# Kernel tuning notes

Hardware: AMD Instinct MI355X
Metric: run time of the kernel (lower is better)

The kernel has to match this reference:

```python
import jax, jax.numpy as jnp
import numpy as np
from jax import lax

ALPHA = 100.0      # SuperSpike surrogate slope (LIFParameters alpha)
DT = 1e-3          # norse default dt
TAU_SYN_INV = 200.0
TAU_MEM_INV = 100.0
V_TH = 1.0

@jax.custom_vjp
def superspike(x):
    return (x > 0).astype(x.dtype)

def _ss_fwd(x):
    return (x > 0).astype(x.dtype), x

def _ss_bwd(x, g):
    return (g / (ALPHA * jnp.abs(x) + 1.0) ** 2,)

superspike.defvjp(_ss_fwd, _ss_bwd)

def lif_step(inp, v, i):
    # norse lif_step: decay v/i, spike on v_decayed - v_th, reset, then add input current
    v_dec = v + DT * TAU_MEM_INV * (-v + i)
    i_dec = i * (1.0 - DT * TAU_SYN_INV)
    z = superspike(v_dec - V_TH)
    v_new = (1.0 - z) * v_dec  # v_reset = 0
    i_new = i_dec + inp
    return z, v_new, i_new

def li_step(inp, v, i):
    # leaky integrator readout (LILinearCell): returns membrane voltage
    v_new = v + DT * TAU_MEM_INV * (-v + i)
    i_new = i * (1.0 - DT * TAU_SYN_INV) + inp
    return v_new, v_new, i_new

def conv2d(x, w, b):
    y = lax.conv_general_dilated(x, w, (1, 1), 'VALID',
                                 dimension_numbers=('NCHW', 'OIHW', 'NCHW'))
    return y + b[None, :, None, None]

def maxpool2(x):
    return lax.reduce_window(x, -jnp.inf, lax.max, (1, 1, 2, 2), (1, 1, 2, 2), 'VALID')

def setup_inputs() -> dict:
    key = jax.random.key(0)
    ks = jax.random.split(key, 9)
    T, B, C, H = 16, 64, 3, 64
    feats = int(((H - 4) / 2 - 4) / 2)  # 13
    def unif(k, shape, fan_in):
        bound = 1.0 / np.sqrt(fan_in)
        return jax.random.uniform(k, shape, jnp.float32, -bound, bound)
    return {
        'x':  jax.random.normal(ks[0], (T, B, C, H, H), jnp.float32),
        'w1': unif(ks[1], (32, C, 5, 5), C * 25),
        'b1': unif(ks[2], (32,), C * 25),
        'w2': unif(ks[3], (64, 32, 5, 5), 32 * 25),
        'b2': unif(ks[4], (64,), 32 * 25),
        'wf': unif(ks[5], (1024, feats * feats * 64), feats * feats * 64),
        'bf': unif(ks[6], (1024,), feats * feats * 64),
        'wo': unif(ks[7], (10, 1024), 1024),
        'bo': unif(ks[8], (10,), 1024),
    }

def reference(x, w1, b1, w2, b2, wf, bf, wo, bo):
    T, B, C, H, _ = x.shape
    h1 = H - 4           # conv1 out spatial
    p1 = h1 // 2         # pool1
    h2 = p1 - 4          # conv2 out spatial
    p2 = h2 // 2         # pool2 (== features)
    dtype = x.dtype
    zeros = lambda s: jnp.zeros(s, dtype)
    carry0 = (zeros((B, 32, h1, h1)), zeros((B, 32, h1, h1)),   # lif0 v, i
              zeros((B, 64, h2, h2)), zeros((B, 64, h2, h2)),   # lif1 v, i
              zeros((B, 1024)), zeros((B, 1024)),               # lif2 v, i
              zeros((B, 10)), zeros((B, 10)))                   # out  v, i

    def step(carry, xt):
        v0, i0, v1, i1, v2, i2, vo, io = carry
        z = conv2d(xt, w1, b1)
        z, v0, i0 = lif_step(z, v0, i0)
        z = maxpool2(z)
        z = 10.0 * conv2d(z, w2, b2)
        z, v1, i1 = lif_step(z, v1, i1)
        z = maxpool2(z)
        z = z.reshape(B, -1)
        z = z @ wf.T + bf
        z, v2, i2 = lif_step(z, v2, i2)
        inp = jax.nn.relu(z) @ wo.T + bo
        v, vo, io = li_step(inp, vo, io)
        return (v0, i0, v1, i1, v2, i2, vo, io), v

    _, voltages = lax.scan(step, carry0, x)
    return voltages  # [T, B, 10]
```

## Files before the change

kernel.cpp:

```cpp
#include <hip/hip_runtime.h>

typedef __attribute__((ext_vector_type(8))) short short8v;
typedef __attribute__((ext_vector_type(4))) float f32x4;

#define DT_TM 0.1f
#define SYN_DEC 0.8f
#define TT 16
#define BB 64
#define FCK 10816

#define BO_S1   ((size_t)0)
#define BO_S2   ((size_t)29491200)
#define BO_S3   ((size_t)51642368)
#define BO_PART ((size_t)55836672)
#define BO_WH2  BO_PART
#define BO_WL2  (BO_PART + 102400)
#define BO_AFW  (BO_PART + 204800)
#define BO_WHF  ((size_t)72613888)
#define BO_WLF  ((size_t)94765056)
#define BIG_NEED ((size_t)116916224)

#define FO_S1   ((size_t)0)
#define FO_S2   ((size_t)29491200)
#define FO_S3   ((size_t)40566784)
#define FO_PART ((size_t)44761088)
#define FO_V2   ((size_t)51576832)
#define FO_I2   ((size_t)51838976)
#define FO_WH2  FO_PART
#define FO_WL2  (FO_PART + 102400)

__device__ __forceinline__ unsigned short bf16_rne(float f) {
  unsigned int u = __float_as_uint(f);
  return (unsigned short)((u + 0x7FFFu + ((u >> 16) & 1u)) >> 16);
}

__global__ __launch_bounds__(256) void k0_prep(
    const float* __restrict__ w2, unsigned short* __restrict__ whi,
    unsigned short* __restrict__ wlo) {
  int e = blockIdx.x * 256 + threadIdx.x;
  if (e >= 25 * 64 * 32) return;
  int kk = e >> 11;
  int rem = e & 2047;
  int oc = rem >> 5, c = rem & 31;
  float w = w2[(size_t)(oc * 32 + c) * 25 + kk];
  unsigned short hi = bf16_rne(w);
  float fhi = __uint_as_float((unsigned int)hi << 16);
  unsigned short lo = bf16_rne(w - fhi);
  whi[e] = hi;
  wlo[e] = lo;
}

__global__ __launch_bounds__(256) void k0b_wf(
    const float* __restrict__ wf, unsigned short* __restrict__ whiF,
    unsigned short* __restrict__ wloF) {
  size_t e = (size_t)blockIdx.x * 256 + threadIdx.x;
  if (e >= (size_t)1024 * FCK) return;
  float w = wf[e];
  unsigned short hi = bf16_rne(w);
  float fhi = __uint_as_float((unsigned int)hi << 16);
  whiF[e] = hi;
  wloF[e] = bf16_rne(w - fhi);
}

__global__ __launch_bounds__(256) void k0w_prep(
    const float* __restrict__ w1, unsigned short* __restrict__ afw) {
  int e = blockIdx.x * 256 + threadIdx.x;
  if (e >= 9216) return;
  int i = e & 7, l = (e >> 3) & 63, f = e >> 9;
  int sp = f % 3, ks = (f / 3) % 3, mt = f / 9;
  int oc = mt * 16 + (l & 15);
  int tap = (l >> 4) * 8 + i;
  unsigned short out = 0;
  int ky = tap / 6, kx = tap - 6 * ky;
  if (tap < 30 && kx < 5) {
    float v = w1[(oc * 3 + ks) * 25 + ky * 5 + kx];
    unsigned short h = bf16_rne(v);
    if (sp == 0) out = h;
    else {
      float r1 = v - __uint_as_float((unsigned int)h << 16);
      unsigned short m = bf16_rne(r1);
      if (sp == 1) out = m;
      else out = bf16_rne(r1 - __uint_as_float((unsigned int)m << 16));
    }
  }
  afw[e] = out;
}

#define MFMA_BF16 __builtin_amdgcn_mfma_f32_16x16x32_bf16

__global__ __launch_bounds__(256) void k1_mfma(
    const float* __restrict__ x, const unsigned short* __restrict__ afw,
    const float* __restrict__ b1, unsigned char* __restrict__ s1) {
  __shared__ unsigned int Hp[2][18 * 81];
  __shared__ unsigned int Mp[2][18 * 81];
  __shared__ unsigned int Lp[2][18 * 81];
  const int s = blockIdx.x;
  const int b = blockIdx.y;
  const int tid = threadIdx.x;
  const int w = tid >> 6, l = tid & 63;
  const int n = l & 15, tg = l >> 4;
  const int xpix = 16 * w + n;
  const int xcl = (xpix < 60) ? xpix : 59;
  const bool storer = ((n & 1) == 0) && (xpix < 60);

  short8v aw[2][3][3];
#pragma unroll
  for (int mt = 0; mt < 2; ++mt)
#pragma unroll
    for (int ks = 0; ks < 3; ++ks)
#pragma unroll
      for (int sp = 0; sp < 3; ++sp)
        aw[mt][ks][sp] =
            *(const short8v*)(afw + (((mt * 3 + ks) * 3 + sp) * 64 + l) * 8);

  f32x4 bias0 = *(const f32x4*)&b1[tg * 4];
  f32x4 bias1 = *(const f32x4*)&b1[16 + tg * 4];

  int poff[4];
#pragma unroll
  for (int i = 0; i < 4; ++i) {
    int tap = tg * 8 + 2 * i;
    int ky = tap / 6, kx = tap - 6 * ky;
    if (tap >= 30) { ky = 4; kx = 0; }
    poff[i] = ky * 81 + kx;
  }

  const int jrow0 = tid >> 5, jcp0 = tid & 31;
  const int jrow1 = (tid + 256) >> 5;
  const int jrow2 = (tid + 512) >> 5;
  const bool job2 = tid < 64;
  const int slan = (l & 32) | ((l + 1) & 31);

  float vst[2][2][4], ist[2][2][4];
#pragma unroll
  for (int a = 0; a < 2; ++a)
#pragma unroll
    for (int m = 0; m < 2; ++m)
#pragma unroll
      for (int r = 0; r < 4; ++r) { vst[a][m][r] = 0.f; ist[a][m][r] = 0.f; }

  float2 pf0, pf1, pf2;

  auto phaseA = [&](int t) {
    const float* xp = x + ((size_t)(t * BB + b)) * 12288 + (size_t)(2 * s) * 64;
    {
      int c = jrow0 / 6, r = jrow0 - 6 * c;
      pf0 = *(const float2*)(xp + c * 4096 + r * 64 + 2 * jcp0);
    }
    {
      int c = jrow1 / 6, r = jrow1 - 6 * c;
      pf1 = *(const float2*)(xp + c * 4096 + r * 64 + 2 * jcp0);
    }
    if (job2) {
      int c = jrow2 / 6, r = jrow2 - 6 * c;
      pf2 = *(const float2*)(xp + c * 4096 + r * 64 + 2 * jcp0);
    }
  };

  auto phaseB = [&](int bfi) {
    unsigned int* H = Hp[bfi];
    unsigned int* M = Mp[bfi];
    unsigned int* L = Lp[bfi];
#pragma unroll
    for (int j = 0; j < 3; ++j) {
      if (j == 2 && !job2) break;
      float2 v2 = (j == 0) ? pf0 : (j == 1) ? pf1 : pf2;
      int row = (j == 0) ? jrow0 : (j == 1) ? jrow1 : jrow2;
      int cp = jcp0;
      unsigned int h0 = bf16_rne(v2.x);
      float r0 = v2.x - __uint_as_float(h0 << 16);
      unsigned int m0 = bf16_rne(r0);
      unsigned int l0 = bf16_rne(r0 - __uint_as_float(m0 << 16));
      unsigned int h1 = bf16_rne(v2.y);
      float r1 = v2.y - __uint_as_float(h1 << 16);
      unsigned int m1 = bf16_rne(r1);
      unsigned int l1 = bf16_rne(r1 - __uint_as_float(m1 << 16));
      unsigned int hm0 = h0 | (m0 << 16);
      unsigned int hmN = (unsigned int)__shfl((int)hm0, slan);
      unsigned int lN  = (unsigned int)__shfl((int)l0, slan);
      int d = row * 81 + 2 * cp;
      H[d]     = h0 | (h1 << 16);
      H[d + 1] = h1 | (hmN << 16);
      M[d]     = m0 | (m1 << 16);
      M[d + 1] = m1 | (hmN & 0xffff0000u);
      L[d]     = l0 | (l1 << 16);
      L[d + 1] = l1 | (lN << 16);
    }
  };

  phaseA(0);
  phaseB(0);
  __syncthreads();

  for (int t = 0; t < TT; ++t) {
    const int cur = t & 1;
    if (t + 1 < TT) phaseA(t + 1);

    const unsigned int* H = Hp[cur];
    const unsigned int* M = Mp[cur];
    const unsigned int* L = Lp[cur];

    unsigned int pk[2];
#pragma unroll
    for (int nt = 0; nt < 2; ++nt) {
      f32x4 acc0 = (f32x4){0.f, 0.f, 0.f, 0.f};
      f32x4 acc1 = (f32x4){0.f, 0.f, 0.f, 0.f};
#pragma unroll
      for (int ks = 0; ks < 3; ++ks) {
        const int base = (ks * 6 + nt) * 81 + xcl;
        union { unsigned int u[4]; short8v v; } fH, fM, fL;
#pragma unroll
        for (int i = 0; i < 4; ++i) {
          fH.u[i] = H[base + poff[i]];
          fM.u[i] = M[base + poff[i]];
          fL.u[i] = L[base + poff[i]];
        }
        acc0 = MFMA_BF16(aw[0][ks][2], fH.v, acc0, 0, 0, 0);
        acc1 = MFMA_BF16(aw[1][ks][2], fH.v, acc1, 0, 0, 0);
        acc0 = MFMA_BF16(aw[0][ks][1], fM.v, acc0, 0, 0, 0);
        acc1 = MFMA_BF16(aw[1][ks][1], fM.v, acc1, 0, 0, 0);
        acc0 = MFMA_BF16(aw[0][ks][0], fL.v, acc0, 0, 0, 0);
        acc1 = MFMA_BF16(aw[1][ks][0], fL.v, acc1, 0, 0, 0);
        acc0 = MFMA_BF16(aw[0][ks][1], fH.v, acc0, 0, 0, 0);
        acc1 = MFMA_BF16(aw[1][ks][1], fH.v, acc1, 0, 0, 0);
        acc0 = MFMA_BF16(aw[0][ks][0], fM.v, acc0, 0, 0, 0);
        acc1 = MFMA_BF16(aw[1][ks][0], fM.v, acc1, 0, 0, 0);
        acc0 = MFMA_BF16(aw[0][ks][0], fH.v, acc0, 0, 0, 0);
        acc1 = MFMA_BF16(aw[1][ks][0], fH.v, acc1, 0, 0, 0);
      }
      unsigned int nib0 = 0, nib1 = 0;
#pragma unroll
      for (int r = 0; r < 4; ++r) {
        float inp = acc0[r] + bias0[r];
        float vd = vst[nt][0][r] + DT_TM * (ist[nt][0][r] - vst[nt][0][r]);
        float id = SYN_DEC * ist[nt][0][r];
        bool z = vd > 1.0f;
        vst[nt][0][r] = z ? 0.f : vd;
        ist[nt][0][r] = id + inp;
        nib0 |= (z ? 1u : 0u) << r;

        float inp1 = acc1[r] + bias1[r];
        float vd1 = vst[nt][1][r] + DT_TM * (ist[nt][1][r] - vst[nt][1][r]);
        float id1 = SYN_DEC * ist[nt][1][r];
        bool z1 = vd1 > 1.0f;
        vst[nt][1][r] = z1 ? 0.f : vd1;
        ist[nt][1][r] = id1 + inp1;
        nib1 |= (z1 ? 1u : 0u) << r;
      }
      pk[nt] = nib0 | (nib1 << 4);
    }
    unsigned int pr = pk[0] | pk[1];
    unsigned int pc = pr | __shfl_xor(pr, 1);
    if (storer) {
      size_t base =
          (((size_t)(t * BB + b)) * 900 + (size_t)s * 30 + (xpix >> 1)) * 32 +
          tg * 4;
      unsigned int lo = pc & 0xFu, hi = (pc >> 4) & 0xFu;
      *(unsigned int*)&s1[base] =
          (lo & 1u) | ((lo & 2u) << 7) | ((lo & 4u) << 14) | ((lo & 8u) << 21);
      *(unsigned int*)&s1[base + 16] =
          (hi & 1u) | ((hi & 2u) << 7) | ((hi & 4u) << 14) | ((hi & 8u) << 21);
    }
    if (t + 1 < TT) {
      phaseB((t + 1) & 1);
      __syncthreads();
    }
  }
}

__global__ __launch_bounds__(256) void k1_conv1(
    const float* __restrict__ x, const float* __restrict__ w1,
    const float* __restrict__ b1, unsigned char* __restrict__ s1) {
  __shared__ float xs[3 * 64 * 68];
  const int oc = blockIdx.x;
  const int b  = blockIdx.y;
  const int tid = threadIdx.x;
  const bool valid = tid < 225;
  const int py0 = (tid / 15) * 2;
  const int px0 = (tid % 15) * 2;
  const int br = 2 * py0;
  const int bc = 2 * px0;

  float v[16], cur[16];
#pragma unroll
  for (int j = 0; j < 16; ++j) { v[j] = 0.f; cur[j] = 0.f; }
  const float bias = b1[oc];

  for (int t = 0; t < TT; ++t) {
    const float* xp = x + ((size_t)(t * BB + b)) * 12288;
#pragma unroll
    for (int k = 0; k < 12; ++k) {
      int e = tid + k * 256;
      int row = e >> 4, c4 = e & 15;
      ((float4*)xs)[row * 17 + c4] = ((const float4*)xp)[e];
    }
    __syncthreads();

    if (valid) {
      float acc[4][4];
#pragma unroll
      for (int r = 0; r < 4; ++r)
#pragma unroll
        for (int s = 0; s < 4; ++s) acc[r][s] = 0.f;

#pragma unroll
      for (int c = 0; c < 3; ++c) {
        const float* wp = w1 + (oc * 3 + c) * 25;
        float wv[25];
#pragma unroll
        for (int j = 0; j < 25; ++j) wv[j] = wp[j];
#pragma unroll
        for (int ri = 0; ri < 8; ++ri) {
          const float* rowp = &xs[(c * 64 + br + ri) * 68 + bc];
          float4 ra = *(const float4*)rowp;
          float4 rb = *(const float4*)(rowp + 4);
          float row[8] = {ra.x, ra.y, ra.z, ra.w, rb.x, rb.y, rb.z, rb.w};
#pragma unroll
          for (int r = 0; r < 4; ++r) {
            int ky = ri - r;
            if (ky >= 0 && ky < 5) {
#pragma unroll
              for (int kx = 0; kx < 5; ++kx) {
                float w = wv[ky * 5 + kx];
#pragma unroll
                for (int s = 0; s < 4; ++s) acc[r][s] += w * row[s + kx];
              }
            }
          }
        }
      }

      unsigned char pz00 = 0, pz01 = 0, pz10 = 0, pz11 = 0;
#pragma unroll
      for (int r = 0; r < 4; ++r)
#pragma unroll
        for (int s = 0; s < 4; ++s) {
          int j = r * 4 + s;
          float vd = v[j] + DT_TM * (cur[j] - v[j]);
          float id = SYN_DEC * cur[j];
          float inp = acc[r][s] + bias;
          bool z = vd > 1.0f;
          v[j] = z ? 0.f : vd;
          cur[j] = id + inp;
          if (z) {
            if (r < 2) { if (s < 2) pz00 = 1; else pz01 = 1; }
            else       { if (s < 2) pz10 = 1; else pz11 = 1; }
          }
        }
      size_t pixb = ((size_t)(t * BB + b)) * 900;
      s1[(pixb + (size_t)py0 * 30 + px0) * 32 + oc]           = pz00;
      s1[(pixb + (size_t)py0 * 30 + px0 + 1) * 32 + oc]       = pz01;
      s1[(pixb + (size_t)(py0 + 1) * 30 + px0) * 32 + oc]     = pz10;
      s1[(pixb + (size_t)(py0 + 1) * 30 + px0 + 1) * 32 + oc] = pz11;
    }
    __syncthreads();
  }
}

__device__ __forceinline__ void k2_stage_load(
    const unsigned char* __restrict__ s1, unsigned int (&pf)[12],
    int t, int b, int y0, int inRows) {
  const int tid = threadIdx.x;
  const unsigned char* sp =
      s1 + (((size_t)(t * BB + b)) * 900 + (size_t)y0 * 30) * 32;
  const int nelem = inRows * 240;
#pragma unroll
  for (int i = 0; i < 12; ++i) {
    int e = tid + i * 256;
    if (e < nelem) pf[i] = *(const unsigned int*)(sp + (size_t)e * 4);
  }
}

__device__ __forceinline__ void k2_stage_write(
    unsigned short* sl, const unsigned int (&pf)[12], int inRows) {
  const int tid = threadIdx.x;
  const int nelem = inRows * 240;
#pragma unroll
  for (int i = 0; i < 12; ++i) {
    int e = tid + i * 256;
    if (e < nelem) {
      unsigned int w = pf[i];
      unsigned int lo = ((w & 0xFFu) ? 0x3F80u : 0u) |
                        ((w & 0xFF00u) ? 0x3F800000u : 0u);
      unsigned int hi = ((w & 0xFF0000u) ? 0x3F80u : 0u) |
                        ((w & 0xFF000000u) ? 0x3F800000u : 0u);
      ((unsigned int*)sl)[e * 2]     = lo;
      ((unsigned int*)sl)[e * 2 + 1] = hi;
    }
  }
}

template<typename ST>
__device__ __forceinline__ void k2_pool(
    ST* __restrict__ s2, const unsigned char* zbuf, int t, int b, int y0, int R) {
  const int tid = threadIdx.x;
  const int prr = R >> 1;
  const int pcount = prr * 13 * 64;
  ST* s2p = s2 + ((size_t)(t * BB + b)) * 64 * 169;
  const int gpy0 = y0 >> 1;
  const ST one = (ST)((sizeof(ST) == 2) ? 0x3F80 : 1);
  for (int e = tid; e < pcount; e += 256) {
    int oc = e & 63, pp = e >> 6;
    int ppy = pp / 13, ppx = pp - ppy * 13;
    int base = (2 * ppy * 26 + 2 * ppx) * 68 + oc;
    unsigned char z = (unsigned char)(zbuf[base] | zbuf[base + 68] |
                      zbuf[base + 26 * 68] | zbuf[base + 26 * 68 + 68]);
    s2p[(size_t)oc * 169 + (gpy0 + ppy) * 13 + ppx] = z ? one : (ST)0;
  }
}

template<int NT>
__device__ __forceinline__ void k2_wave(
    const unsigned short* sl, float* Vst, float* Ist, unsigned char* zbuf,
    const unsigned short* __restrict__ whi, const unsigned short* __restrict__ wlo,
    const float* __restrict__ b2, int og, int q, int n, int ntstart, int npos) {
  int baddr[NT], pcl[NT];
  f32x4 acc[2][NT];
#pragma unroll
  for (int j = 0; j < NT; ++j) {
    int pl = (ntstart + j) * 16 + n;
    if (pl > npos - 1) pl = npos - 1;
    pcl[j] = pl;
    int ry = pl / 26, xx = pl - ry * 26;
    baddr[j] = (ry * 30 + xx) * 32 + q * 8;
    acc[0][j] = (f32x4){0.f, 0.f, 0.f, 0.f};
    acc[1][j] = (f32x4){0.f, 0.f, 0.f, 0.f};
  }
  const int abase = (og * 32 + n) * 32 + q * 8;
#pragma unroll 5
  for (int kk = 0; kk < 25; ++kk) {
    const int ky = kk / 5, kx = kk - (kk / 5) * 5;
    const int off = (ky * 30 + kx) * 32;
    short8v ah0 = *(const short8v*)(whi + kk * 2048 + abase);
    short8v al0 = *(const short8v*)(wlo + kk * 2048 + abase);
    short8v ah1 = *(const short8v*)(whi + kk * 2048 + abase + 512);
    short8v al1 = *(const short8v*)(wlo + kk * 2048 + abase + 512);
#pragma unroll
    for (int j = 0; j < NT; ++j) {
      short8v bv = *(const short8v*)(sl + baddr[j] + off);
      acc[0][j] = MFMA_BF16(al0, bv, acc[0][j], 0, 0, 0);
      acc[0][j] = MFMA_BF16(ah0, bv, acc[0][j], 0, 0, 0);
      acc[1][j] = MFMA_BF16(al1, bv, acc[1][j], 0, 0, 0);
      acc[1][j] = MFMA_BF16(ah1, bv, acc[1][j], 0, 0, 0);
    }
  }
  const f32x4 bias0 = *(const f32x4*)&b2[og * 32 + q * 4];
  const f32x4 bias1 = *(const f32x4*)&b2[og * 32 + 16 + q * 4];
#pragma unroll
  for (int j = 0; j < NT; ++j) {
    int p = pcl[j];
#pragma unroll
    for (int mi = 0; mi < 2; ++mi) {
      int sidx = p * 68 + og * 32 + mi * 16 + q * 4;
      f32x4 v4 = *(f32x4*)&Vst[sidx];
      f32x4 i4 = *(f32x4*)&Ist[sidx];
      f32x4 bia = mi ? bias1 : bias0;
      f32x4 a = acc[mi][j];
      unsigned char zr[4];
#pragma unroll
      for (int r = 0; r < 4; ++r) {
        float vd = v4[r] + DT_TM * (i4[r] - v4[r]);
        float id = SYN_DEC * i4[r];
        float inp = 10.f * (a[r] + bia[r]);
        bool z = vd > 1.0f;
        v4[r] = z ? 0.f : vd;
        i4[r] = id + inp;
        zr[r] = z ? 1 : 0;
      }
      *(f32x4*)&Vst[sidx] = v4;
      *(f32x4*)&Ist[sidx] = i4;
      *(uchar4*)&zbuf[sidx] = make_uchar4(zr[0], zr[1], zr[2], zr[3]);
    }
  }
}

template<typename ST>
__global__ __launch_bounds__(256) void k2_mfma_l(
    const unsigned char* __restrict__ s1, const unsigned short* __restrict__ whi,
    const unsigned short* __restrict__ wlo, const float* __restrict__ b2,
    ST* __restrict__ s2) {
  __shared__ unsigned short sl[12 * 30 * 32];
  __shared__ float Vst[208 * 68];
  __shared__ float Ist[208 * 68];
  __shared__ unsigned char zbuf[208 * 68];
  const int quad = blockIdx.x, b = blockIdx.y;
  const int tid = threadIdx.x;
  const int wid = tid >> 6, l = tid & 63;
  const int og = wid & 1, nc = wid >> 1;
  const int q = l >> 4, n = l & 15;
  const int y0 = (quad == 0) ? 0 : (2 + quad * 6);
  const int R  = (quad == 0) ? 8 : 6;
  const int inRows = R + 4;
  const int npos = R * 26;

  for (int e = tid; e < 208 * 68; e += 256) { Vst[e] = 0.f; Ist[e] = 0.f; }

  unsigned int pf[12];
  k2_stage_load(s1, pf, 0, b, y0, inRows);
  k2_stage_write(sl, pf, inRows);
  __syncthreads();

  for (int t = 0; t < TT; ++t) {
    if (t + 1 < TT) k2_stage_load(s1, pf, t + 1, b, y0, inRows);

    if (quad == 0) {
      if (nc == 0) k2_wave<7>(sl, Vst, Ist, zbuf, whi, wlo, b2, og, q, n, 0, npos);
      else         k2_wave<6>(sl, Vst, Ist, zbuf, whi, wlo, b2, og, q, n, 7, npos);
    } else {
      k2_wave<5>(sl, Vst, Ist, zbuf, whi, wlo, b2, og, q, n, nc * 5, npos);
    }
    __syncthreads();

    k2_pool<ST>(s2, zbuf, t, b, y0, R);
    if (t + 1 < TT) k2_stage_write(sl, pf, inRows);
    __syncthreads();
  }
}

__global__ __launch_bounds__(512) void k3g_fc(
    const unsigned short* __restrict__ s2,
    const unsigned short* __restrict__ whiF,
    const unsigned short* __restrict__ wloF,
    float* __restrict__ part) {
  __shared__ __align__(16) unsigned short As[128][72];
  __shared__ __align__(16) unsigned short Bh[128][72];
  __shared__ __align__(16) unsigned short Bl[128][72];
  const int tid = threadIdx.x;
  const int w = tid >> 6, l = tid & 63;
  const int mh = w & 1, nq = w >> 1;
  const int lr = l & 15, lk = l >> 4;
  const int n0 = blockIdx.x * 128, m0 = blockIdx.y * 128;
  const int ks = blockIdx.z;
  const int s_begin = (169 * ks) >> 2, s_end = (169 * (ks + 1)) >> 2;

  const int arow = tid >> 2, aseg = tid & 3;
  const unsigned short* ap = s2 + (size_t)(m0 + arow) * FCK + aseg * 16;
  unsigned short* aq = &As[0][0] + arow * 72 + aseg * 16;
  const int barr = tid >> 8, brem = tid & 255;
  const int bn = brem >> 1, bhalf = brem & 1;
  const unsigned short* bp =
      (barr ? wloF : whiF) + (size_t)(n0 + bn) * FCK + bhalf * 32;
  unsigned short* bq = (barr ? &Bl[0][0] : &Bh[0][0]) + bn * 72 + bhalf * 32;

  f32x4 acc[4][2];
#pragma unroll
  for (int mt = 0; mt < 4; ++mt)
#pragma unroll
    for (int nt = 0; nt < 2; ++nt) acc[mt][nt] = (f32x4){0.f, 0.f, 0.f, 0.f};

  for (int s = s_begin; s < s_end; ++s) {
    const size_t k0 = (size_t)s * 64;
    short8v a0 = *(const short8v*)(ap + k0);
    short8v a1 = *(const short8v*)(ap + k0 + 8);
    short8v b0 = *(const short8v*)(bp + k0);
    short8v b1 = *(const short8v*)(bp + k0 + 8);
    short8v b2v = *(const short8v*)(bp + k0 + 16);
    short8v b3 = *(const short8v*)(bp + k0 + 24);
    __syncthreads();
    *(short8v*)(aq)      = a0;
    *(short8v*)(aq + 8)  = a1;
    *(short8v*)(bq)      = b0;
    *(short8v*)(bq + 8)  = b1;
    *(short8v*)(bq + 16) = b2v;
    *(short8v*)(bq + 24) = b3;
    __syncthreads();
#pragma unroll
    for (int kt = 0; kt < 2; ++kt) {
      short8v bh0 = *(const short8v*)&Bh[nq * 32 + lr][kt * 32 + lk * 8];
      short8v bh1 = *(const short8v*)&Bh[nq * 32 + 16 + lr][kt * 32 + lk * 8];
      short8v bl0 = *(const short8v*)&Bl[nq * 32 + lr][kt * 32 + lk * 8];
      short8v bl1 = *(const short8v*)&Bl[nq * 32 + 16 + lr][kt * 32 + lk * 8];
#pragma unroll
      for (int mt = 0; mt < 4; ++mt) {
        short8v af = *(const short8v*)&As[mh * 64 + mt * 16 + lr][kt * 32 + lk * 8];
        acc[mt][0] = MFMA_BF16(af, bh0, acc[mt][0], 0, 0, 0);
        acc[mt][0] = MFMA_BF16(af, bl0, acc[mt][0], 0, 0, 0);
        acc[mt][1] = MFMA_BF16(af, bh1, acc[mt][1], 0, 0, 0);
        acc[mt][1] = MFMA_BF16(af, bl1, acc[mt][1], 0, 0, 0);
      }
    }
  }
  float* pp = part + ((size_t)ks << 20);
#pragma unroll
  for (int mt = 0; mt < 4; ++mt)
#pragma unroll
    for (int nt = 0; nt < 2; ++nt) {
      int mrow = m0 + mh * 64 + mt * 16 + lk * 4;
      int ncol = n0 + nq * 32 + nt * 16 + lr;
#pragma unroll
      for (int r = 0; r < 4; ++r)
        pp[(size_t)(mrow + r) * 1024 + ncol] = acc[mt][nt][r];
    }
}

__global__ __launch_bounds__(256) void k3r_lif2(
    const float* __restrict__ part, const float* __restrict__ bf,
    float* __restrict__ s3) {
  int e = blockIdx.x * 256 + threadIdx.x;
  int n = e & 1023;
  const float bias = bf[n];
  float v = 0.f, cur = 0.f;
  for (int t = 0; t < TT; ++t) {
    size_t idx = ((size_t)(t * BB) << 10) + e;
    float g = part[idx] + part[idx + (1u << 20)] +
              part[idx + (2u << 20)] + part[idx + (3u << 20)] + bias;
    float vd = v + DT_TM * (cur - v);
    float id = SYN_DEC * cur;
    bool sp = vd > 1.0f;
    v = sp ? 0.f : vd;
    cur = id + g;
    s3[(size_t)t * 65536 + e] = sp ? 1.f : 0.f;
  }
}

__global__ __launch_bounds__(256) void k3a_fc(
    const unsigned char* __restrict__ s2, const float* __restrict__ wf,
    float* __restrict__ part, int t) {
  __shared__ float As[16][68];
  __shared__ float Bs[16][68];
  const int nt = blockIdx.x;
  const int ks = blockIdx.y;
  const int tid = threadIdx.x;
  const int N0 = nt * 64;
  const int kbase = ks * 416;
  const unsigned char* A = s2 + (size_t)t * BB * FCK;

  const int lm = tid >> 2;
  const int kq = tid & 3;
  const int m0 = (tid >> 4) << 2;
  const int n0 = (tid & 15) << 2;

  float acc[4][4];
#pragma unroll
  for (int i = 0; i < 4; ++i)
#pragma unroll
    for (int j = 0; j < 4; ++j) acc[i][j] = 0.f;

  for (int step = 0; step < 26; ++step) {
    int k0 = kbase + step * 16;
    uchar4 a4 = *(const uchar4*)&A[(size_t)lm * FCK + k0 + kq * 4];
    float4 b4 = *(const float4*)&wf[(size_t)(N0 + lm) * FCK + k0 + kq * 4];
    __syncthreads();
    As[kq * 4 + 0][lm] = (float)a4.x;
    As[kq * 4 + 1][lm] = (float)a4.y;
    As[kq * 4 + 2][lm] = (float)a4.z;
    As[kq * 4 + 3][lm] = (float)a4.w;
    Bs[kq * 4 + 0][lm] = b4.x;
    Bs[kq * 4 + 1][lm] = b4.y;
    Bs[kq * 4 + 2][lm] = b4.z;
    Bs[kq * 4 + 3][lm] = b4.w;
    __syncthreads();
#pragma unroll
    for (int kk = 0; kk < 16; ++kk) {
      float4 av = *(const float4*)&As[kk][m0];
      float4 bv = *(const float4*)&Bs[kk][n0];
      float a0 = av.x, a1 = av.y, a2 = av.z, a3 = av.w;
      acc[0][0] += a0 * bv.x; acc[0][1] += a0 * bv.y; acc[0][2] += a0 * bv.z; acc[0][3] += a0 * bv.w;
      acc[1][0] += a1 * bv.x; acc[1][1] += a1 * bv.y; acc[1][2] += a1 * bv.z; acc[1][3] += a1 * bv.w;
      acc[2][0] += a2 * bv.x; acc[2][1] += a2 * bv.y; acc[2][2] += a2 * bv.z; acc[2][3] += a2 * bv.w;
      acc[3][0] += a3 * bv.x; acc[3][1] += a3 * bv.y; acc[3][2] += a3 * bv.z; acc[3][3] += a3 * bv.w;
    }
  }
#pragma unroll
  for (int i = 0; i < 4; ++i)
#pragma unroll
    for (int j = 0; j < 4; ++j)
      part[((size_t)(ks * 64 + m0 + i)) * 1024 + N0 + n0 + j] = acc[i][j];
}

__global__ __launch_bounds__(256) void k3b_lif2(
    const float* __restrict__ part, const float* __restrict__ bf,
    float* __restrict__ v2, float* __restrict__ i2,
    float* __restrict__ s3, int t) {
  int e = blockIdx.x * 256 + threadIdx.x;
  int n = e & 1023;
  float s = 0.f;
#pragma unroll
  for (int ks = 0; ks < 26; ++ks) s += part[(size_t)ks * 65536 + e];
  float z = s + bf[n];
  float vv = v2[e], ii = i2[e];
  float vd = vv + DT_TM * (ii - vv);
  float id = SYN_DEC * ii;
  bool sp = vd > 1.0f;
  v2[e] = sp ? 0.f : vd;
  i2[e] = id + z;
  s3[(size_t)t * 65536 + e] = sp ? 1.f : 0.f;
}

__global__ __launch_bounds__(320) void k4_out(
    const float* __restrict__ s3, const float* __restrict__ wo,
    const float* __restrict__ bo, float* __restrict__ out) {
  const int b = blockIdx.x;
  const int g = threadIdx.x >> 5;
  const int l = threadIdx.x & 31;
  float vv = 0.f, ii = 0.f;
  const float bg = bo[g];
  for (int t = 0; t < TT; ++t) {
    const float* zp = s3 + ((size_t)t * BB + b) * 1024;
    const float* wp = wo + g * 1024;
    float p = 0.f;
#pragma unroll 8
    for (int j = l; j < 1024; j += 32) p += zp[j] * wp[j];
#pragma unroll
    for (int off = 16; off; off >>= 1) p += __shfl_down(p, off, 32);
    float inp = p + bg;
    float vn = vv + DT_TM * (ii - vv);
    if (l == 0) out[(size_t)(t * BB + b) * 10 + g] = vn;
    ii = SYN_DEC * ii + inp;
    vv = vn;
  }
}

extern "C" void kernel_launch(void* const* d_in, const int* in_sizes, int n_in,
                              void* d_out, int out_size, void* d_ws, size_t ws_size,
                              hipStream_t stream) {
  (void)in_sizes; (void)n_in; (void)out_size;
  const float* x  = (const float*)d_in[0];
  const float* w1 = (const float*)d_in[1];
  const float* b1 = (const float*)d_in[2];
  const float* w2 = (const float*)d_in[3];
  const float* b2 = (const float*)d_in[4];
  const float* wf = (const float*)d_in[5];
  const float* bf = (const float*)d_in[6];
  const float* wo = (const float*)d_in[7];
  const float* bo = (const float*)d_in[8];
  float* out = (float*)d_out;
  char* ws = (char*)d_ws;

  if (ws_size >= BIG_NEED) {
    unsigned char*  s1   = (unsigned char*)(ws + BO_S1);
    unsigned short* s2   = (unsigned short*)(ws + BO_S2);
    float*          s3   = (float*)(ws + BO_S3);
    float*          part = (float*)(ws + BO_PART);
    unsigned short* wh2  = (unsigned short*)(ws + BO_WH2);
    unsigned short* wl2  = (unsigned short*)(ws + BO_WL2);
    unsigned short* afw  = (unsigned short*)(ws + BO_AFW);
    unsigned short* whiF = (unsigned short*)(ws + BO_WHF);
    unsigned short* wloF = (unsigned short*)(ws + BO_WLF);

    k0_prep<<<dim3(200), 256, 0, stream>>>(w2, wh2, wl2);
    k0w_prep<<<dim3(36), 256, 0, stream>>>(w1, afw);
    k0b_wf<<<dim3(43264), 256, 0, stream>>>(wf, whiF, wloF);
    k1_mfma<<<dim3(30, 64), 256, 0, stream>>>(x, afw, b1, s1);
    k2_mfma_l<unsigned short><<<dim3(4, 64), 256, 0, stream>>>(
        s1, wh2, wl2, b2, s2);
    k3g_fc<<<dim3(8, 8, 4), 512, 0, stream>>>(s2, whiF, wloF, part);
    k3r_lif2<<<dim3(256), 256, 0, stream>>>(part, bf, s3);
    k4_out<<<dim3(64), 320, 0, stream>>>(s3, wo, bo, out);
  } else {
    unsigned char*  s1   = (unsigned char*)(ws + FO_S1);
    unsigned char*  s2   = (unsigned char*)(ws + FO_S2);
    float*          s3   = (float*)(ws + FO_S3);
    float*          part = (float*)(ws + FO_PART);
    float*          v2   = (float*)(ws + FO_V2);
    float*          i2   = (float*)(ws + FO_I2);
    unsigned short* wh2  = (unsigned short*)(ws + FO_WH2);
    unsigned short* wl2  = (unsigned short*)(ws + FO_WL2);

    hipMemsetAsync(v2, 0, 2 * 65536 * sizeof(float), stream);
    k0_prep<<<dim3(200), 256, 0, stream>>>(w2, wh2, wl2);
    k1_conv1<<<dim3(32, 64), 256, 0, stream>>>(x, w1, b1, s1);
    k2_mfma_l<unsigned char><<<dim3(4, 64), 256, 0, stream>>>(s1, wh2, wl2, b2, s2);
    for (int t = 0; t < TT; ++t) {
      k3a_fc<<<dim3(16, 26), 256, 0, stream>>>(s2, wf, part, t);
      k3b_lif2<<<dim3(256), 256, 0, stream>>>(part, bf, v2, i2, s3, t);
    }
    k4_out<<<dim3(64), 320, 0, stream>>>(s3, wo, bo, out);
  }
}
```

Baseline: 496.5 us.

## Split conv2 output-channel halves across twice as many waves in k2

The conv2+LIF kernel now launches 512 threads per block instead of 256. Each wave handles one 16-channel half (mi) of its 32-channel group rather than both, which halves the accumulators and MFMA chain per wave. Staging loads, pooling and init loops are restrided to the larger block. The aim is more waves to hide latency and fewer registers per thread, at the cost of each wave reloading the shared B operand, so LDS reads double.

```diff
diff --git a/kernel.cpp b/kernel.cpp
--- a/kernel.cpp
+++ b/kernel.cpp
@@ -358,26 +358,26 @@
 }
 
 __device__ __forceinline__ void k2_stage_load(
-    const unsigned char* __restrict__ s1, unsigned int (&pf)[12],
+    const unsigned char* __restrict__ s1, unsigned int (&pf)[6],
     int t, int b, int y0, int inRows) {
   const int tid = threadIdx.x;
   const unsigned char* sp =
       s1 + (((size_t)(t * BB + b)) * 900 + (size_t)y0 * 30) * 32;
   const int nelem = inRows * 240;
 #pragma unroll
-  for (int i = 0; i < 12; ++i) {
-    int e = tid + i * 256;
+  for (int i = 0; i < 6; ++i) {
+    int e = tid + i * 512;
     if (e < nelem) pf[i] = *(const unsigned int*)(sp + (size_t)e * 4);
   }
 }
 
 __device__ __forceinline__ void k2_stage_write(
-    unsigned short* sl, const unsigned int (&pf)[12], int inRows) {
+    unsigned short* sl, const unsigned int (&pf)[6], int inRows) {
   const int tid = threadIdx.x;
   const int nelem = inRows * 240;
 #pragma unroll
-  for (int i = 0; i < 12; ++i) {
-    int e = tid + i * 256;
+  for (int i = 0; i < 6; ++i) {
+    int e = tid + i * 512;
     if (e < nelem) {
       unsigned int w = pf[i];
       unsigned int lo = ((w & 0xFFu) ? 0x3F80u : 0u) |
@@ -399,7 +399,7 @@
   ST* s2p = s2 + ((size_t)(t * BB + b)) * 64 * 169;
   const int gpy0 = y0 >> 1;
   const ST one = (ST)((sizeof(ST) == 2) ? 0x3F80 : 1);
-  for (int e = tid; e < pcount; e += 256) {
+  for (int e = tid; e < pcount; e += 512) {
     int oc = e & 63, pp = e >> 6;
     int ppy = pp / 13, ppx = pp - ppy * 13;
     int base = (2 * ppy * 26 + 2 * ppx) * 68 + oc;
@@ -413,9 +413,10 @@
 __device__ __forceinline__ void k2_wave(
     const unsigned short* sl, float* Vst, float* Ist, unsigned char* zbuf,
     const unsigned short* __restrict__ whi, const unsigned short* __restrict__ wlo,
-    const float* __restrict__ b2, int og, int q, int n, int ntstart, int npos) {
+    const float* __restrict__ b2, int og, int mi, int q, int n,
+    int ntstart, int npos) {
   int baddr[NT], pcl[NT];
-  f32x4 acc[2][NT];
+  f32x4 acc[NT];
 #pragma unroll
   for (int j = 0; j < NT; ++j) {
     int pl = (ntstart + j) * 16 + n;
@@ -423,59 +424,49 @@
     pcl[j] = pl;
     int ry = pl / 26, xx = pl - ry * 26;
     baddr[j] = (ry * 30 + xx) * 32 + q * 8;
-    acc[0][j] = (f32x4){0.f, 0.f, 0.f, 0.f};
-    acc[1][j] = (f32x4){0.f, 0.f, 0.f, 0.f};
-  }
-  const int abase = (og * 32 + n) * 32 + q * 8;
+    acc[j] = (f32x4){0.f, 0.f, 0.f, 0.f};
+  }
+  const int abase = (og * 32 + n) * 32 + q * 8 + mi * 512;
 #pragma unroll 5
   for (int kk = 0; kk < 25; ++kk) {
     const int ky = kk / 5, kx = kk - (kk / 5) * 5;
     const int off = (ky * 30 + kx) * 32;
-    short8v ah0 = *(const short8v*)(whi + kk * 2048 + abase);
-    short8v al0 = *(const short8v*)(wlo + kk * 2048 + abase);
-    short8v ah1 = *(const short8v*)(whi + kk * 2048 + abase + 512);
-    short8v al1 = *(const short8v*)(wlo + kk * 2048 + abase + 512);
+    short8v ah = *(const short8v*)(whi + kk * 2048 + abase);
+    short8v al = *(const short8v*)(wlo + kk * 2048 + abase);
 #pragma unroll
     for (int j = 0; j < NT; ++j) {
       short8v bv = *(const short8v*)(sl + baddr[j] + off);
-      acc[0][j] = MFMA_BF16(al0, bv, acc[0][j], 0, 0, 0);
-      acc[0][j] = MFMA_BF16(ah0, bv, acc[0][j], 0, 0, 0);
-      acc[1][j] = MFMA_BF16(al1, bv, acc[1][j], 0, 0, 0);
-      acc[1][j] = MFMA_BF16(ah1, bv, acc[1][j], 0, 0, 0);
-    }
-  }
-  const f32x4 bias0 = *(const f32x4*)&b2[og * 32 + q * 4];
-  const f32x4 bias1 = *(const f32x4*)&b2[og * 32 + 16 + q * 4];
+      acc[j] = MFMA_BF16(al, bv, acc[j], 0, 0, 0);
+      acc[j] = MFMA_BF16(ah, bv, acc[j], 0, 0, 0);
+    }
+  }
+  const f32x4 bia = *(const f32x4*)&b2[og * 32 + mi * 16 + q * 4];
 #pragma unroll
   for (int j = 0; j < NT; ++j) {
     int p = pcl[j];
-#pragma unroll
-    for (int mi = 0; mi < 2; ++mi) {
-      int sidx = p * 68 + og * 32 + mi * 16 + q * 4;
-      f32x4 v4 = *(f32x4*)&Vst[sidx];
-      f32x4 i4 = *(f32x4*)&Ist[sidx];
-      f32x4 bia = mi ? bias1 : bias0;
-      f32x4 a = acc[mi][j];
-      unsigned char zr[4];
-#pragma unroll
-      for (int r = 0; r < 4; ++r) {
-        float vd = v4[r] + DT_TM * (i4[r] - v4[r]);
-        float id = SYN_DEC * i4[r];
-        float inp = 10.f * (a[r] + bia[r]);
-        bool z = vd > 1.0f;
-        v4[r] = z ? 0.f : vd;
-        i4[r] = id + inp;
-        zr[r] = z ? 1 : 0;
-      }
-      *(f32x4*)&Vst[sidx] = v4;
-      *(f32x4*)&Ist[sidx] = i4;
-      *(uchar4*)&zbuf[sidx] = make_uchar4(zr[0], zr[1], zr[2], zr[3]);
-    }
+    int sidx = p * 68 + og * 32 + mi * 16 + q * 4;
+    f32x4 v4 = *(f32x4*)&Vst[sidx];
+    f32x4 i4 = *(f32x4*)&Ist[sidx];
+    f32x4 a = acc[j];
+    unsigned char zr[4];
+#pragma unroll
+    for (int r = 0; r < 4; ++r) {
+      float vd = v4[r] + DT_TM * (i4[r] - v4[r]);
+      float id = SYN_DEC * i4[r];
+      float inp = 10.f * (a[r] + bia[r]);
+      bool z = vd > 1.0f;
+      v4[r] = z ? 0.f : vd;
+      i4[r] = id + inp;
+      zr[r] = z ? 1 : 0;
+    }
+    *(f32x4*)&Vst[sidx] = v4;
+    *(f32x4*)&Ist[sidx] = i4;
+    *(uchar4*)&zbuf[sidx] = make_uchar4(zr[0], zr[1], zr[2], zr[3]);
   }
 }
 
 template<typename ST>
-__global__ __launch_bounds__(256) void k2_mfma_l(
+__global__ __launch_bounds__(512) void k2_mfma_l(
     const unsigned char* __restrict__ s1, const unsigned short* __restrict__ whi,
     const unsigned short* __restrict__ wlo, const float* __restrict__ b2,
     ST* __restrict__ s2) {
@@ -486,16 +477,16 @@
   const int quad = blockIdx.x, b = blockIdx.y;
   const int tid = threadIdx.x;
   const int wid = tid >> 6, l = tid & 63;
-  const int og = wid & 1, nc = wid >> 1;
+  const int og = wid & 1, mi = (wid >> 1) & 1, nc = wid >> 2;
   const int q = l >> 4, n = l & 15;
   const int y0 = (quad == 0) ? 0 : (2 + quad * 6);
   const int R  = (quad == 0) ? 8 : 6;
   const int inRows = R + 4;
   const int npos = R * 26;
 
-  for (int e = tid; e < 208 * 68; e += 256) { Vst[e] = 0.f; Ist[e] = 0.f; }
-
-  unsigned int pf[12];
+  for (int e = tid; e < 208 * 68; e += 512) { Vst[e] = 0.f; Ist[e] = 0.f; }
+
+  unsigned int pf[6];
   k2_stage_load(s1, pf, 0, b, y0, inRows);
   k2_stage_write(sl, pf, inRows);
   __syncthreads();
@@ -504,10 +495,12 @@
     if (t + 1 < TT) k2_stage_load(s1, pf, t + 1, b, y0, inRows);
 
     if (quad == 0) {
-      if (nc == 0) k2_wave<7>(sl, Vst, Ist, zbuf, whi, wlo, b2, og, q, n, 0, npos);
-      else         k2_wave<6>(sl, Vst, Ist, zbuf, whi, wlo, b2, og, q, n, 7, npos);
+      if (nc == 0)
+        k2_wave<7>(sl, Vst, Ist, zbuf, whi, wlo, b2, og, mi, q, n, 0, npos);
+      else
+        k2_wave<6>(sl, Vst, Ist, zbuf, whi, wlo, b2, og, mi, q, n, 7, npos);
     } else {
-      k2_wave<5>(sl, Vst, Ist, zbuf, whi, wlo, b2, og, q, n, nc * 5, npos);
+      k2_wave<5>(sl, Vst, Ist, zbuf, whi, wlo, b2, og, mi, q, n, nc * 5, npos);
     }
     __syncthreads();
 
@@ -742,7 +735,7 @@
     k0w_prep<<<dim3(36), 256, 0, stream>>>(w1, afw);
     k0b_wf<<<dim3(43264), 256, 0, stream>>>(wf, whiF, wloF);
     k1_mfma<<<dim3(30, 64), 256, 0, stream>>>(x, afw, b1, s1);
-    k2_mfma_l<unsigned short><<<dim3(4, 64), 256, 0, stream>>>(
+    k2_mfma_l<unsigned short><<<dim3(4, 64), 512, 0, stream>>>(
         s1, wh2, wl2, b2, s2);
     k3g_fc<<<dim3(8, 8, 4), 512, 0, stream>>>(s2, whiF, wloF, part);
     k3r_lif2<<<dim3(256), 256, 0, stream>>>(part, bf, s3);
@@ -760,7 +753,7 @@
     hipMemsetAsync(v2, 0, 2 * 65536 * sizeof(float), stream);
     k0_prep<<<dim3(200), 256, 0, stream>>>(w2, wh2, wl2);
     k1_conv1<<<dim3(32, 64), 256, 0, stream>>>(x, w1, b1, s1);
-    k2_mfma_l<unsigned char><<<dim3(4, 64), 256, 0, stream>>>(s1, wh2, wl2, b2, s2);
+    k2_mfma_l<unsigned char><<<dim3(4, 64), 512, 0, stream>>>(s1, wh2, wl2, b2, s2);
     for (int t = 0; t < TT; ++t) {
       k3a_fc<<<dim3(16, 26), 256, 0, stream>>>(s2, wf, part, t);
       k3b_lif2<<<dim3(256), 256, 0, stream>>>(part, bf, v2, i2, s3, t);
```

New measurement: 444.2 us (median of 2 runs). -10.5%, faster.
